# Kernel optimization log

Hardware: AMD Instinct MI355X
Metric: run time of the kernel (lower is better)

## Reference

```python
import jax, jax.numpy as jnp
import numpy as np

TOP_K = 2

def setup_inputs() -> dict:
    key = jax.random.key(0)
    ks = jax.random.split(key, 5)
    B, S, D, E, R, H = 4, 2048, 1024, 8, 128, 4096
    s = 0.02
    return {
        "hidden_states": jax.random.normal(ks[0], (B, S, D), jnp.float32),
        "w_route": jax.random.normal(ks[1], (E, D, R), jnp.float32) * s,
        "w3": jax.random.normal(ks[2], (E, D, H), jnp.float32) * s,
        "wr2h": jax.random.normal(ks[3], (E, R, H), jnp.float32) * s,
        "wh2d": jax.random.normal(ks[4], (E, H, D), jnp.float32) * s,
    }

def reference(hidden_states, w_route, w3, wr2h, wh2d):
    B, S, D = hidden_states.shape
    E = w_route.shape[0]
    x = hidden_states.reshape(-1, D)                      # [N, D]
    N = x.shape[0]
    # per-expert routing activations (also reused as w1_state inside experts)
    acts = jnp.einsum('nd,edr->ner', x, w_route)          # [N, E, R]
    norms = jnp.linalg.norm(acts, axis=-1)                # [N, E] router logits
    probs = jax.nn.softmax(norms.astype(jnp.float32), axis=-1)
    topw, sel = jax.lax.top_k(probs, TOP_K)               # [N, k]
    topw = topw / topw.sum(axis=-1, keepdims=True)
    topw = topw.astype(x.dtype)
    # dense combine weights: routing weight if expert selected, else 0
    combine = jnp.zeros((N, E), x.dtype).at[jnp.arange(N)[:, None], sel].add(topw)
    out = jnp.zeros_like(x)
    for e in range(E):  # fixed small expert count
        h = (x @ w3[e]) * jax.nn.silu(acts[:, e, :] @ wr2h[e])  # [N, H]
        out = out + (h @ wh2d[e]) * combine[:, e:e + 1]
    final = out.reshape(B, S, D)
    # load balancing loss on the router logits (expert_act_norms)
    mask = jax.nn.one_hot(sel, E, dtype=jnp.float32)      # [N, k, E]
    tokens_per_expert = mask.mean(axis=0)                 # [k, E]
    router_prob_per_expert = probs.mean(axis=0)           # [E]
    bl_loss = jnp.sum(tokens_per_expert * router_prob_per_expert[None, :]) * E
    return final, norms, bl_loss
```

## Files before the change

### kernel.cpp

```cpp
#include <hip/hip_runtime.h>


#define DEV static __device__ __forceinline__

typedef float  f32x4  __attribute__((ext_vector_type(4)));
typedef __bf16 bf16x8 __attribute__((ext_vector_type(8)));

DEV unsigned short f2bf(float f) {
  union { float f; unsigned u; } v; v.f = f;
  unsigned r = v.u + 0x7fffu + ((v.u >> 16) & 1u);
  return (unsigned short)(r >> 16);
}
DEV float bf2f(unsigned short b) {
  union { unsigned u; float f; } v; v.u = ((unsigned)b) << 16;
  return v.f;
}

DEV void gll16(const void* g, void* l) {
  __builtin_amdgcn_global_load_lds(
      (const __attribute__((address_space(1))) unsigned int*)g,
      (__attribute__((address_space(3))) unsigned int*)l, 16, 0, 0);
}

DEV f32x4 mfma16(bf16x8 a, bf16x8 b, f32x4 c) {
  return __builtin_amdgcn_mfma_f32_16x16x32_bf16(a, b, c, 0, 0, 0);
}

DEV int xcd_swz_gen(int bid, int nwg) {
  int x = bid & 7, o = bid >> 3;
  int q = nwg >> 3, r = nwg & 7;
  return (x < r ? x * (q + 1) : r * (q + 1) + (x - r) * q) + o;
}

DEV bf16x8 frag_read(const unsigned short* lds, int row, int kb) {
  int off = row * 128 + ((kb * 2) ^ ((row & 7) << 4));
  return *(const bf16x8*)((const char*)lds + off);
}

DEV void stage_linear(const unsigned short* base, size_t pitch, int k0,
                      unsigned short* lds, int tid) {
  int wq = tid >> 6, lane = tid & 63;
#pragma unroll
  for (int i = 0; i < 4; ++i) {
    int s = wq * 256 + i * 64 + lane;
    int row = s >> 3, b = s & 7;
    int bb = b ^ (row & 7);
    const unsigned short* g = base + (size_t)row * pitch + (size_t)(k0 + bb * 8);
    gll16(g, lds + (size_t)(wq * 256 + i * 64) * 8);
  }
}

DEV void stage_l256(const unsigned short* base, size_t pitch, int k0,
                    unsigned short* lds, int tid) {
  int wq = tid >> 6, lane = tid & 63;
#pragma unroll
  for (int i = 0; i < 4; ++i) {
    int sb = wq * 256 + i * 64;
    int s = sb + lane;
    int row = s >> 3, b = s & 7;
    int bb = b ^ (row & 7);
    gll16(base + (size_t)row * pitch + (size_t)(k0 + bb * 8),
          lds + (size_t)sb * 8);
  }
}
DEV void stage_g256(const unsigned short* base, size_t pitch, size_t colOff,
                    int k0, const int* toks, unsigned short* lds, int tid) {
  int wq = tid >> 6, lane = tid & 63;
#pragma unroll
  for (int i = 0; i < 4; ++i) {
    int sb = wq * 256 + i * 64;
    int s = sb + lane;
    int row = s >> 3, b = s & 7;
    int bb = b ^ (row & 7);
    gll16(base + (size_t)toks[row] * pitch + colOff + (size_t)(k0 + bb * 8),
          lds + (size_t)sb * 8);
  }
}
DEV void stage_l128(const unsigned short* base, size_t pitch, int k0,
                    unsigned short* lds, int tid) {
  int wq = tid >> 6, lane = tid & 63;
#pragma unroll
  for (int i = 0; i < 2; ++i) {
    int sb = wq * 128 + i * 64;
    int s = sb + lane;
    int row = s >> 3, b = s & 7;
    int bb = b ^ (row & 7);
    gll16(base + (size_t)row * pitch + (size_t)(k0 + bb * 8),
          lds + (size_t)sb * 8);
  }
}

DEV void mfma_block(const unsigned short* A, const unsigned short* B,
                    f32x4 (&acc)[4][4], int wm, int wn, int lg, int lc) {
#pragma unroll
  for (int ks = 0; ks < 2; ++ks) {
    int kb = ks * 32 + lg * 8;
    bf16x8 af[4], bff[4];
#pragma unroll
    for (int i = 0; i < 4; ++i) {
      af[i]  = frag_read(A, wm * 64 + i * 16 + lc, kb);
      bff[i] = frag_read(B, wn * 64 + i * 16 + lc, kb);
    }
#pragma unroll
    for (int mf = 0; mf < 4; ++mf)
#pragma unroll
      for (int nf = 0; nf < 4; ++nf)
        acc[mf][nf] = mfma16(af[mf], bff[nf], acc[mf][nf]);
  }
}
DEV void mfma256x256(const unsigned short* A, const unsigned short* B,
                     f32x4 (&acc)[8][4], int wm, int wn, int lg, int lc) {
#pragma unroll
  for (int ks = 0; ks < 2; ++ks) {
    int kb = ks * 32 + lg * 8;
    bf16x8 af[8], bff[4];
#pragma unroll
    for (int i = 0; i < 8; ++i) af[i] = frag_read(A, wm * 128 + i * 16 + lc, kb);
#pragma unroll
    for (int i = 0; i < 4; ++i) bff[i] = frag_read(B, wn * 64 + i * 16 + lc, kb);
#pragma unroll
    for (int mf = 0; mf < 8; ++mf)
#pragma unroll
      for (int nf = 0; nf < 4; ++nf)
        acc[mf][nf] = mfma16(af[mf], bff[nf], acc[mf][nf]);
  }
}
DEV void mfma256x128(const unsigned short* A, const unsigned short* B,
                     f32x4 (&acc)[8][2], int wm, int wn, int lg, int lc) {
#pragma unroll
  for (int ks = 0; ks < 2; ++ks) {
    int kb = ks * 32 + lg * 8;
    bf16x8 af[8], bff[2];
#pragma unroll
    for (int i = 0; i < 8; ++i) af[i] = frag_read(A, wm * 128 + i * 16 + lc, kb);
#pragma unroll
    for (int i = 0; i < 2; ++i) bff[i] = frag_read(B, wn * 32 + i * 16 + lc, kb);
#pragma unroll
    for (int mf = 0; mf < 8; ++mf)
#pragma unroll
      for (int nf = 0; nf < 2; ++nf)
        acc[mf][nf] = mfma16(af[mf], bff[nf], acc[mf][nf]);
  }
}


__global__ __launch_bounds__(256) void k_cast_x(const float* __restrict__ x,
    unsigned short* __restrict__ xh, unsigned short* __restrict__ xl) {
  int stride = gridDim.x * blockDim.x;
  for (int i = blockIdx.x * blockDim.x + threadIdx.x; i < 8192 * 1024 / 4;
       i += stride) {
    float4 v = ((const float4*)x)[i];
    ushort4 h, l;
    h.x = f2bf(v.x); l.x = f2bf(v.x - bf2f(h.x));
    h.y = f2bf(v.y); l.y = f2bf(v.y - bf2f(h.y));
    h.z = f2bf(v.z); l.z = f2bf(v.z - bf2f(h.z));
    h.w = f2bf(v.w); l.w = f2bf(v.w - bf2f(h.w));
    ((ushort4*)xh)[i] = h;
    ((ushort4*)xl)[i] = l;
  }
}

__global__ void k_zero(int* cnt, float* probsum) {
  int t = threadIdx.x;
  if (t < 16) cnt[t] = 0;
  if (t < 8)  probsum[t] = 0.f;
}

__global__ __launch_bounds__(256) void k_transp(const float* __restrict__ src,
    unsigned short* __restrict__ dst, int K, int N) {
  int ntn = N >> 6;
  int kt = blockIdx.x / ntn, nt = blockIdx.x % ntn;
  int e = blockIdx.y;
  __shared__ float tl[64][65];
  const float* s = src + (size_t)e * K * N;
  unsigned short* d = dst + (size_t)e * N * K;
  int tid = threadIdx.x;
  int c4 = (tid & 15) * 4, rr = tid >> 4;
#pragma unroll
  for (int p = 0; p < 4; ++p) {
    int row = rr + p * 16;
    float4 v = *(const float4*)(s + (size_t)(kt * 64 + row) * N + nt * 64 + c4);
    tl[row][c4] = v.x; tl[row][c4 + 1] = v.y;
    tl[row][c4 + 2] = v.z; tl[row][c4 + 3] = v.w;
  }
  __syncthreads();
#pragma unroll
  for (int p = 0; p < 4; ++p) {
    int n = rr + p * 16;
    ushort4 o;
    o.x = f2bf(tl[c4 + 0][n]); o.y = f2bf(tl[c4 + 1][n]);
    o.z = f2bf(tl[c4 + 2][n]); o.w = f2bf(tl[c4 + 3][n]);
    *(ushort4*)(d + (size_t)(nt * 64 + n) * K + kt * 64 + c4) = o;
  }
}

__global__ __launch_bounds__(256) void k_transp_split(const float* __restrict__ src,
    unsigned short* __restrict__ dh, unsigned short* __restrict__ dl, int K, int N) {
  int ntn = N >> 6;
  int kt = blockIdx.x / ntn, nt = blockIdx.x % ntn;
  int e = blockIdx.y;
  __shared__ float tl[64][65];
  const float* s = src + (size_t)e * K * N;
  size_t dbase = (size_t)e * N * K;
  int tid = threadIdx.x;
  int c4 = (tid & 15) * 4, rr = tid >> 4;
#pragma unroll
  for (int p = 0; p < 4; ++p) {
    int row = rr + p * 16;
    float4 v = *(const float4*)(s + (size_t)(kt * 64 + row) * N + nt * 64 + c4);
    tl[row][c4] = v.x; tl[row][c4 + 1] = v.y;
    tl[row][c4 + 2] = v.z; tl[row][c4 + 3] = v.w;
  }
  __syncthreads();
#pragma unroll
  for (int p = 0; p < 4; ++p) {
    int n = rr + p * 16;
    ushort4 oh, ol;
#pragma unroll
    for (int i = 0; i < 4; ++i) {
      float v = tl[c4 + i][n];
      unsigned short hh = f2bf(v);
      unsigned short ll = f2bf(v - bf2f(hh));
      ((unsigned short*)&oh)[i] = hh;
      ((unsigned short*)&ol)[i] = ll;
    }
    *(ushort4*)(dh + dbase + (size_t)(nt * 64 + n) * K + kt * 64 + c4) = oh;
    *(ushort4*)(dl + dbase + (size_t)(nt * 64 + n) * K + kt * 64 + c4) = ol;
  }
}

__global__ __launch_bounds__(256) void k_route_gemm(
    const unsigned short* __restrict__ xh, const unsigned short* __restrict__ xl,
    const unsigned short* __restrict__ wrh_t, const unsigned short* __restrict__ wrl_t,
    unsigned short* __restrict__ acts, float* __restrict__ norms_out) {
  __shared__ __align__(16) unsigned short Ah[128 * 64], Al[128 * 64];
  __shared__ __align__(16) unsigned short Bh[128 * 64], Bl[128 * 64];
  __shared__ float ssq_s[128][2];
  int tid = threadIdx.x;
  int mt = blockIdx.x, e = blockIdx.y;
  int wq = tid >> 6, lane = tid & 63;
  int wm = wq >> 1, wn = wq & 1, lg = lane >> 4, lc = lane & 15;
  f32x4 acc[4][4] = {};
  const unsigned short* ah_src = xh + (size_t)mt * 128 * 1024;
  const unsigned short* al_src = xl + (size_t)mt * 128 * 1024;
  const unsigned short* bh_src = wrh_t + (size_t)e * 128 * 1024;
  const unsigned short* bl_src = wrl_t + (size_t)e * 128 * 1024;
  for (int kt = 0; kt < 16; ++kt) {
    int k0 = kt * 64;
    stage_linear(ah_src, 1024, k0, Ah, tid);
    stage_linear(al_src, 1024, k0, Al, tid);
    stage_linear(bh_src, 1024, k0, Bh, tid);
    stage_linear(bl_src, 1024, k0, Bl, tid);
    __syncthreads();
#pragma unroll
    for (int ks = 0; ks < 2; ++ks) {
      int kb = ks * 32 + lg * 8;
      bf16x8 ahf[4], alf[4], bhf[4], blf[4];
#pragma unroll
      for (int i = 0; i < 4; ++i) {
        ahf[i] = frag_read(Ah, wm * 64 + i * 16 + lc, kb);
        alf[i] = frag_read(Al, wm * 64 + i * 16 + lc, kb);
        bhf[i] = frag_read(Bh, wn * 64 + i * 16 + lc, kb);
        blf[i] = frag_read(Bl, wn * 64 + i * 16 + lc, kb);
      }
#pragma unroll
      for (int mf = 0; mf < 4; ++mf)
#pragma unroll
        for (int nf = 0; nf < 4; ++nf) {
          acc[mf][nf] = mfma16(ahf[mf], bhf[nf], acc[mf][nf]);
          acc[mf][nf] = mfma16(alf[mf], bhf[nf], acc[mf][nf]);
          acc[mf][nf] = mfma16(ahf[mf], blf[nf], acc[mf][nf]);
        }
    }
    __syncthreads();
  }
  float ssq[4][4];
#pragma unroll
  for (int mf = 0; mf < 4; ++mf)
#pragma unroll
    for (int r = 0; r < 4; ++r) ssq[mf][r] = 0.f;
#pragma unroll
  for (int mf = 0; mf < 4; ++mf)
#pragma unroll
    for (int nf = 0; nf < 4; ++nf)
#pragma unroll
      for (int r = 0; r < 4; ++r) {
        float v = acc[mf][nf][r];
        int row = wm * 64 + mf * 16 + lg * 4 + r;
        int col = wn * 64 + nf * 16 + lc;
        acts[(size_t)(mt * 128 + row) * 1024 + e * 128 + col] = f2bf(v);
        ssq[mf][r] += v * v;
      }
#pragma unroll
  for (int mf = 0; mf < 4; ++mf)
#pragma unroll
    for (int r = 0; r < 4; ++r) {
      float s = ssq[mf][r];
      s += __shfl_xor(s, 1); s += __shfl_xor(s, 2);
      s += __shfl_xor(s, 4); s += __shfl_xor(s, 8);
      if (lc == 0) ssq_s[wm * 64 + mf * 16 + lg * 4 + r][wn] = s;
    }
  __syncthreads();
  if (tid < 128) {
    float s = ssq_s[tid][0] + ssq_s[tid][1];
    norms_out[(size_t)(mt * 128 + tid) * 8 + e] = sqrtf(s);
  }
}

__global__ __launch_bounds__(256) void k_router(const float* __restrict__ norms,
    float* __restrict__ topw, int* __restrict__ sel,
    int* __restrict__ cnt, float* __restrict__ probsum) {
  __shared__ float ps_s[8];
  __shared__ int cnt_s[16];
  int tid = threadIdx.x;
  if (tid < 8)  ps_s[tid] = 0.f;
  if (tid < 16) cnt_s[tid] = 0;
  __syncthreads();
  int n = blockIdx.x * 256 + tid;
  float p[8], mx = -3.4e38f;
#pragma unroll
  for (int e = 0; e < 8; ++e) { p[e] = norms[(size_t)n * 8 + e]; mx = fmaxf(mx, p[e]); }
  float s = 0.f;
#pragma unroll
  for (int e = 0; e < 8; ++e) { p[e] = __expf(p[e] - mx); s += p[e]; }
  float inv = 1.f / s;
  int i1 = 0; float v1 = p[0];
#pragma unroll
  for (int e = 1; e < 8; ++e) if (p[e] > v1) { v1 = p[e]; i1 = e; }
  int i2 = -1; float v2 = -1.f;
#pragma unroll
  for (int e = 0; e < 8; ++e) if (e != i1 && p[e] > v2) { v2 = p[e]; i2 = e; }
  float wsum = v1 + v2;
  topw[n * 2 + 0] = v1 / wsum;
  topw[n * 2 + 1] = v2 / wsum;
  sel[n * 2 + 0] = i1;
  sel[n * 2 + 1] = i2;
  atomicAdd(&cnt_s[i1], 1);
  atomicAdd(&cnt_s[8 + i2], 1);
#pragma unroll
  for (int e = 0; e < 8; ++e) atomicAdd(&ps_s[e], p[e] * inv);
  __syncthreads();
  if (tid < 8)  atomicAdd(&probsum[tid], ps_s[tid]);
  if (tid < 16) atomicAdd(&cnt[tid], cnt_s[tid]);
}

__global__ void k_plan(const int* __restrict__ cnt, const float* __restrict__ probsum,
                       int* __restrict__ offs, int* __restrict__ fill,
                       int4* __restrict__ tilemap, float* __restrict__ bl_out) {
  int t = 0;
  for (int k = 0; k < 2; ++k) {
    int pos = 0;
    for (int e = 0; e < 8; ++e) {
      int c = cnt[k * 8 + e];
      offs[k * 8 + e] = pos;
      int ntl = (c + 255) >> 8;
      for (int i = 0; i < ntl; ++i) {
        int rr = c - i * 256; if (rr > 256) rr = 256;
        tilemap[t] = make_int4(e, k * 8192 + pos + i * 256, rr, 0);
        ++t;
      }
      pos += c;
    }
  }
  for (; t < 80; ++t) tilemap[t] = make_int4(0, 0, 0, 0);
  for (int i = 0; i < 16; ++i) fill[i] = 0;
  float bl = 0.f;
  for (int e = 0; e < 8; ++e)
    bl += ((float)(cnt[e] + cnt[8 + e]) / 8192.f) * (probsum[e] / 8192.f);
  *bl_out = bl * 8.f;
}

__global__ __launch_bounds__(256) void k_fill(const int* __restrict__ sel,
    const float* __restrict__ topw, const int* __restrict__ offs,
    int* __restrict__ fill, int* __restrict__ list01, float* __restrict__ wlist) {
  int n = blockIdx.x * 256 + threadIdx.x;
#pragma unroll
  for (int k = 0; k < 2; ++k) {
    int e = sel[n * 2 + k];
    int pos = atomicAdd(&fill[k * 8 + e], 1);
    int idx = k * 8192 + offs[k * 8 + e] + pos;
    list01[idx] = n;
    wlist[idx] = topw[n * 2 + k];
  }
}

__global__ __launch_bounds__(512, 2) void k_gemm1(
    const unsigned short* __restrict__ xh, const unsigned short* __restrict__ acts,
    const unsigned short* __restrict__ w3t, const unsigned short* __restrict__ wr2h_t,
    const int* __restrict__ list, const int4* __restrict__ tilemap, int tile_lo,
    int nt, unsigned short* __restrict__ hbuf) {
  __shared__ __align__(16) unsigned short SA[2][256 * 64];
  __shared__ __align__(16) unsigned short SB[2][128 * 64];
  __shared__ int toks[256];
  int wg = xcd_swz_gen((int)blockIdx.x, nt * 32);
  int tloc = wg >> 5, bn = wg & 31;
  int4 ent = tilemap[tile_lo + tloc];
  int e = ent.x, posbase = ent.y, rows = ent.z;
  if (rows == 0) return;
  int tid = threadIdx.x;
  if (tid < 256) {
    int rr = tid < rows ? tid : rows - 1;
    toks[tid] = list[posbase + rr];
  }
  __syncthreads();
  int wq = tid >> 6, lane = tid & 63;
  int wm = wq >> 2, wn = wq & 3, lg = lane >> 4, lc = lane & 15;
  f32x4 acc_a[8][2] = {}, acc_s[8][2] = {};
  const unsigned short* bsrc  = w3t + ((size_t)e * 4096 + bn * 128) * 1024;
  const unsigned short* b2src = wr2h_t + ((size_t)e * 4096 + bn * 128) * 128;
  stage_g256(xh, 1024, 0, 0, toks, SA[0], tid);
  stage_l128(bsrc, 1024, 0, SB[0], tid);
  __syncthreads();
  int cur = 0;
  for (int kt = 0; kt < 15; ++kt) {
    stage_g256(xh, 1024, 0, (kt + 1) * 64, toks, SA[cur ^ 1], tid);
    stage_l128(bsrc, 1024, (kt + 1) * 64, SB[cur ^ 1], tid);
    mfma256x128(SA[cur], SB[cur], acc_a, wm, wn, lg, lc);
    __syncthreads();
    cur ^= 1;
  }
  stage_g256(acts, 1024, (size_t)e * 128, 0, toks, SA[cur ^ 1], tid);
  stage_l128(b2src, 128, 0, SB[cur ^ 1], tid);
  mfma256x128(SA[cur], SB[cur], acc_a, wm, wn, lg, lc);
  __syncthreads();
  cur ^= 1;
  stage_g256(acts, 1024, (size_t)e * 128, 64, toks, SA[cur ^ 1], tid);
  stage_l128(b2src, 128, 64, SB[cur ^ 1], tid);
  mfma256x128(SA[cur], SB[cur], acc_s, wm, wn, lg, lc);
  __syncthreads();
  cur ^= 1;
  mfma256x128(SA[cur], SB[cur], acc_s, wm, wn, lg, lc);
  size_t hrow0 = (size_t)tloc * 256;
#pragma unroll
  for (int mf = 0; mf < 8; ++mf)
#pragma unroll
    for (int nf = 0; nf < 2; ++nf)
#pragma unroll
      for (int r = 0; r < 4; ++r) {
        int row = wm * 128 + mf * 16 + lg * 4 + r;
        if (row < rows) {
          int col = wn * 32 + nf * 16 + lc;
          float sv = acc_s[mf][nf][r];
          float hv = acc_a[mf][nf][r] * (sv / (1.f + __expf(-sv)));
          hbuf[(hrow0 + row) * 4096 + (size_t)bn * 128 + col] = f2bf(hv);
        }
      }
}

__global__ __launch_bounds__(512, 2) void k_gemm2(
    const unsigned short* __restrict__ hbuf, const unsigned short* __restrict__ wh2dt,
    const int* __restrict__ list, const float* __restrict__ wlist,
    const int4* __restrict__ tilemap, int tile_lo, int nt,
    float* __restrict__ out) {
  __shared__ __align__(16) unsigned short SA[2][256 * 64];
  __shared__ __align__(16) unsigned short SB[2][256 * 64];
  __shared__ int toks[256];
  __shared__ float wr_s[256];
  int wg = xcd_swz_gen((int)blockIdx.x, nt * 4);
  int tloc = wg >> 2, bn = wg & 3;
  int4 ent = tilemap[tile_lo + tloc];
  int e = ent.x, posbase = ent.y, rows = ent.z;
  if (rows == 0) return;
  int tid = threadIdx.x;
  if (tid < 256) {
    int rr = tid < rows ? tid : rows - 1;
    int t = list[posbase + rr];
    toks[tid] = t;
    wr_s[tid] = wlist[posbase + rr];
  }
  __syncthreads();
  int wq = tid >> 6, lane = tid & 63;
  int wm = wq >> 2, wn = wq & 3, lg = lane >> 4, lc = lane & 15;
  f32x4 acc[8][4] = {};
  const unsigned short* asrc = hbuf + (size_t)tloc * 256 * 4096;
  const unsigned short* bsrc = wh2dt + ((size_t)e * 1024 + bn * 256) * 4096;
  stage_l256(asrc, 4096, 0, SA[0], tid);
  stage_l256(bsrc, 4096, 0, SB[0], tid);
  __syncthreads();
  int cur = 0;
  for (int kt = 0; kt < 63; ++kt) {
    stage_l256(asrc, 4096, (kt + 1) * 64, SA[cur ^ 1], tid);
    stage_l256(bsrc, 4096, (kt + 1) * 64, SB[cur ^ 1], tid);
    mfma256x256(SA[cur], SB[cur], acc, wm, wn, lg, lc);
    __syncthreads();
    cur ^= 1;
  }
  mfma256x256(SA[cur], SB[cur], acc, wm, wn, lg, lc);
#pragma unroll
  for (int mf = 0; mf < 8; ++mf)
#pragma unroll
    for (int nf = 0; nf < 4; ++nf)
#pragma unroll
      for (int r = 0; r < 4; ++r) {
        int row = wm * 128 + mf * 16 + lg * 4 + r;
        if (row < rows) {
          int col = wn * 64 + nf * 16 + lc;
          float v = acc[mf][nf][r] * wr_s[row];
          atomicAdd(out + (size_t)toks[row] * 1024 + bn * 256 + col, v);
        }
      }
}


extern "C" void kernel_launch(void* const* d_in, const int* in_sizes, int n_in,
                              void* d_out, int out_size, void* d_ws, size_t ws_size,
                              hipStream_t stream) {
  (void)in_sizes; (void)n_in; (void)out_size;
  const float* x      = (const float*)d_in[0];
  const float* wroute = (const float*)d_in[1];
  const float* w3     = (const float*)d_in[2];
  const float* wr2h   = (const float*)d_in[3];
  const float* wh2d   = (const float*)d_in[4];
  float* out = (float*)d_out;

  char* ws = (char*)d_ws;
  size_t off = 0;
  auto carve = [&](size_t bytes) -> void* {
    void* p = ws + off; off += (bytes + 255) & ~(size_t)255; return p;
  };
  unsigned short* xh     = (unsigned short*)carve((size_t)8192 * 1024 * 2);
  unsigned short* xl     = (unsigned short*)carve((size_t)8192 * 1024 * 2);
  unsigned short* wrh_t  = (unsigned short*)carve((size_t)8 * 128 * 1024 * 2);
  unsigned short* wrl_t  = (unsigned short*)carve((size_t)8 * 128 * 1024 * 2);
  unsigned short* w3t    = (unsigned short*)carve((size_t)8 * 4096 * 1024 * 2);
  unsigned short* wr2h_t = (unsigned short*)carve((size_t)8 * 4096 * 128 * 2);
  unsigned short* wh2dt  = (unsigned short*)carve((size_t)8 * 1024 * 4096 * 2);
  unsigned short* acts   = (unsigned short*)carve((size_t)8192 * 1024 * 2);
  int*   list01 = (int*)carve(2 * 8192 * 4);
  float* wlist  = (float*)carve(2 * 8192 * 4);
  int*   sel    = (int*)carve(8192 * 2 * 4);
  float* topw   = (float*)carve(8192 * 2 * 4);
  int*   ctr    = (int*)carve(8192);
  int* cnt = ctr; int* fill = ctr + 16; int* offs = ctr + 32;
  float* probsum = (float*)(ctr + 48);
  int4* tilemap = (int4*)(ctr + 64);

  size_t avail = ws_size > off ? ws_size - off : 0;
  int tpc = 0;
  const int cands[4] = {80, 40, 20, 10};
  for (int i = 0; i < 4; ++i) {
    if ((size_t)cands[i] * 256 * 4096 * 2 <= avail) { tpc = cands[i]; break; }
  }
  if (!tpc) return;
  unsigned short* hbuf = (unsigned short*)(ws + off);

  float* norms_out = out + 8388608;
  float* bl_out    = out + 8454144;

  hipMemsetAsync(out, 0, (size_t)8388608 * 4, stream);
  k_cast_x<<<2048, 256, 0, stream>>>(x, xh, xl);
  k_zero<<<1, 64, 0, stream>>>(cnt, probsum);
  k_transp<<<dim3(16 * 64, 8), 256, 0, stream>>>(w3, w3t, 1024, 4096);
  k_transp<<<dim3(64 * 16, 8), 256, 0, stream>>>(wh2d, wh2dt, 4096, 1024);
  k_transp<<<dim3(2 * 64, 8), 256, 0, stream>>>(wr2h, wr2h_t, 128, 4096);
  k_transp_split<<<dim3(16 * 2, 8), 256, 0, stream>>>(wroute, wrh_t, wrl_t, 1024, 128);
  k_route_gemm<<<dim3(64, 8), 256, 0, stream>>>(xh, xl, wrh_t, wrl_t, acts, norms_out);
  k_router<<<32, 256, 0, stream>>>(norms_out, topw, sel, cnt, probsum);
  k_plan<<<1, 1, 0, stream>>>(cnt, probsum, offs, fill, tilemap, bl_out);
  k_fill<<<32, 256, 0, stream>>>(sel, topw, offs, fill, list01, wlist);

  int nchunk = (80 + tpc - 1) / tpc;
  for (int c = 0; c < nchunk; ++c) {
    int tile_lo = c * tpc;
    int nt = 80 - tile_lo < tpc ? 80 - tile_lo : tpc;
    k_gemm1<<<nt * 32, 512, 0, stream>>>(
        xh, acts, w3t, wr2h_t, list01, tilemap, tile_lo, nt, hbuf);
    k_gemm2<<<nt * 4, 512, 0, stream>>>(
        hbuf, wh2dt, list01, wlist, tilemap, tile_lo, nt, out);
  }
}
```

Measured before the change: 955.0 us.

## Restructure expert GEMMs into quadrant-interleaved pipelines with fine-grained waitcnt

Rewrites the main loops of both expert GEMM kernels (gated up-projection and down-projection) as an explicit software pipeline. Each tile is split into quadrants whose LDS fragment reads, global-to-LDS stages and MFMA blocks are interleaved. Full __syncthreads are replaced by s_barrier plus manual vmcnt/lgkmcnt waits and s_setprio around the MFMA bursts. The per-warp tile mapping changes to a 2x2 quadrant layout. The goal is to hide global load latency and LDS traffic behind matrix math, at the cost of fragile hand-counted wait counts and more complex scheduling.

```diff
diff --git a/kernel.cpp b/kernel.cpp
--- a/kernel.cpp
+++ b/kernel.cpp
@@ -5,6 +5,10 @@
 
 typedef float  f32x4  __attribute__((ext_vector_type(4)));
 typedef __bf16 bf16x8 __attribute__((ext_vector_type(8)));
+
+#define VMCNT_(n) asm volatile("s_waitcnt vmcnt(" #n ")" ::: "memory")
+#define VMCNT(n) VMCNT_(n)
+#define LGKM0()  asm volatile("s_waitcnt lgkmcnt(0)" ::: "memory")
 
 DEV unsigned short f2bf(float f) {
   union { float f; unsigned u; } v; v.f = f;
@@ -49,47 +53,6 @@
     gll16(g, lds + (size_t)(wq * 256 + i * 64) * 8);
   }
 }
-
-DEV void stage_l256(const unsigned short* base, size_t pitch, int k0,
-                    unsigned short* lds, int tid) {
-  int wq = tid >> 6, lane = tid & 63;
-#pragma unroll
-  for (int i = 0; i < 4; ++i) {
-    int sb = wq * 256 + i * 64;
-    int s = sb + lane;
-    int row = s >> 3, b = s & 7;
-    int bb = b ^ (row & 7);
-    gll16(base + (size_t)row * pitch + (size_t)(k0 + bb * 8),
-          lds + (size_t)sb * 8);
-  }
-}
-DEV void stage_g256(const unsigned short* base, size_t pitch, size_t colOff,
-                    int k0, const int* toks, unsigned short* lds, int tid) {
-  int wq = tid >> 6, lane = tid & 63;
-#pragma unroll
-  for (int i = 0; i < 4; ++i) {
-    int sb = wq * 256 + i * 64;
-    int s = sb + lane;
-    int row = s >> 3, b = s & 7;
-    int bb = b ^ (row & 7);
-    gll16(base + (size_t)toks[row] * pitch + colOff + (size_t)(k0 + bb * 8),
-          lds + (size_t)sb * 8);
-  }
-}
-DEV void stage_l128(const unsigned short* base, size_t pitch, int k0,
-                    unsigned short* lds, int tid) {
-  int wq = tid >> 6, lane = tid & 63;
-#pragma unroll
-  for (int i = 0; i < 2; ++i) {
-    int sb = wq * 128 + i * 64;
-    int s = sb + lane;
-    int row = s >> 3, b = s & 7;
-    int bb = b ^ (row & 7);
-    gll16(base + (size_t)row * pitch + (size_t)(k0 + bb * 8),
-          lds + (size_t)sb * 8);
-  }
-}
-
 DEV void mfma_block(const unsigned short* A, const unsigned short* B,
                     f32x4 (&acc)[4][4], int wm, int wn, int lg, int lc) {
 #pragma unroll
@@ -105,40 +68,6 @@
     for (int mf = 0; mf < 4; ++mf)
 #pragma unroll
       for (int nf = 0; nf < 4; ++nf)
-        acc[mf][nf] = mfma16(af[mf], bff[nf], acc[mf][nf]);
-  }
-}
-DEV void mfma256x256(const unsigned short* A, const unsigned short* B,
-                     f32x4 (&acc)[8][4], int wm, int wn, int lg, int lc) {
-#pragma unroll
-  for (int ks = 0; ks < 2; ++ks) {
-    int kb = ks * 32 + lg * 8;
-    bf16x8 af[8], bff[4];
-#pragma unroll
-    for (int i = 0; i < 8; ++i) af[i] = frag_read(A, wm * 128 + i * 16 + lc, kb);
-#pragma unroll
-    for (int i = 0; i < 4; ++i) bff[i] = frag_read(B, wn * 64 + i * 16 + lc, kb);
-#pragma unroll
-    for (int mf = 0; mf < 8; ++mf)
-#pragma unroll
-      for (int nf = 0; nf < 4; ++nf)
-        acc[mf][nf] = mfma16(af[mf], bff[nf], acc[mf][nf]);
-  }
-}
-DEV void mfma256x128(const unsigned short* A, const unsigned short* B,
-                     f32x4 (&acc)[8][2], int wm, int wn, int lg, int lc) {
-#pragma unroll
-  for (int ks = 0; ks < 2; ++ks) {
-    int kb = ks * 32 + lg * 8;
-    bf16x8 af[8], bff[2];
-#pragma unroll
-    for (int i = 0; i < 8; ++i) af[i] = frag_read(A, wm * 128 + i * 16 + lc, kb);
-#pragma unroll
-    for (int i = 0; i < 2; ++i) bff[i] = frag_read(B, wn * 32 + i * 16 + lc, kb);
-#pragma unroll
-    for (int mf = 0; mf < 8; ++mf)
-#pragma unroll
-      for (int nf = 0; nf < 2; ++nf)
         acc[mf][nf] = mfma16(af[mf], bff[nf], acc[mf][nf]);
   }
 }
@@ -405,46 +334,134 @@
   __syncthreads();
   int wq = tid >> 6, lane = tid & 63;
   int wm = wq >> 2, wn = wq & 3, lg = lane >> 4, lc = lane & 15;
-  f32x4 acc_a[8][2] = {}, acc_s[8][2] = {};
-  const unsigned short* bsrc  = w3t + ((size_t)e * 4096 + bn * 128) * 1024;
-  const unsigned short* b2src = wr2h_t + ((size_t)e * 4096 + bn * 128) * 128;
-  stage_g256(xh, 1024, 0, 0, toks, SA[0], tid);
-  stage_l128(bsrc, 1024, 0, SB[0], tid);
-  __syncthreads();
-  int cur = 0;
-  for (int kt = 0; kt < 15; ++kt) {
-    stage_g256(xh, 1024, 0, (kt + 1) * 64, toks, SA[cur ^ 1], tid);
-    stage_l128(bsrc, 1024, (kt + 1) * 64, SB[cur ^ 1], tid);
-    mfma256x128(SA[cur], SB[cur], acc_a, wm, wn, lg, lc);
-    __syncthreads();
-    cur ^= 1;
-  }
-  stage_g256(acts, 1024, (size_t)e * 128, 0, toks, SA[cur ^ 1], tid);
-  stage_l128(b2src, 128, 0, SB[cur ^ 1], tid);
-  mfma256x128(SA[cur], SB[cur], acc_a, wm, wn, lg, lc);
-  __syncthreads();
-  cur ^= 1;
-  stage_g256(acts, 1024, (size_t)e * 128, 64, toks, SA[cur ^ 1], tid);
-  stage_l128(b2src, 128, 64, SB[cur ^ 1], tid);
-  mfma256x128(SA[cur], SB[cur], acc_s, wm, wn, lg, lc);
-  __syncthreads();
-  cur ^= 1;
-  mfma256x128(SA[cur], SB[cur], acc_s, wm, wn, lg, lc);
+
+  int sa0 = tid, sa1 = tid + 512;
+  int ra0 = sa0 >> 3, ra1 = sa1 >> 3;
+  int ca0 = ((sa0 & 7) ^ (ra0 & 7)) * 8;
+  int ca1 = ((sa1 & 7) ^ (ra1 & 7)) * 8;
+  int tA00 = toks[ra0],      tA01 = toks[128 + ra0];
+  int tA10 = toks[ra1],      tA11 = toks[128 + ra1];
+  int rb = tid >> 3;
+  int cb = ((tid & 7) ^ (rb & 7)) * 8;
+
+  auto stageA = [&](int t, int h, int bi) {
+    unsigned short* d0 = &SA[bi][(size_t)(h * 1024 + sa0) * 8];
+    unsigned short* d1 = &SA[bi][(size_t)(h * 1024 + sa1) * 8];
+    int t0 = h ? tA01 : tA00, t1 = h ? tA11 : tA10;
+    if (t < 16) {
+      int k0 = t * 64;
+      gll16(xh + (size_t)t0 * 1024 + k0 + ca0, d0);
+      gll16(xh + (size_t)t1 * 1024 + k0 + ca1, d1);
+    } else {
+      int k0 = e * 128 + (t - 16) * 64;
+      gll16(acts + (size_t)t0 * 1024 + k0 + ca0, d0);
+      gll16(acts + (size_t)t1 * 1024 + k0 + ca1, d1);
+    }
+  };
+  auto stageB = [&](int t, int h, int bi) {
+    unsigned short* d = &SB[bi][(size_t)(h * 512 + tid) * 8];
+    if (t < 16) {
+      gll16(w3t + ((size_t)e * 4096 + bn * 128 + h * 64 + rb) * 1024 + t * 64 + cb, d);
+    } else {
+      gll16(wr2h_t + ((size_t)e * 4096 + bn * 128 + h * 64 + rb) * 128 +
+                (t - 16) * 64 + cb, d);
+    }
+  };
+
+  f32x4 accm[2][4][2] = {}, accg[2][4][2] = {};
+  bf16x8 af[4][2], bf[2][2];
+
+#define G1_RA(BI, QM)                                                        \
+  _Pragma("unroll") for (int mf = 0; mf < 4; ++mf)                           \
+  _Pragma("unroll") for (int ks = 0; ks < 2; ++ks)                           \
+    af[mf][ks] = frag_read(SA[BI], QM * 128 + wm * 64 + mf * 16 + lc,        \
+                           ks * 32 + lg * 8);
+#define G1_RB(BI, QN)                                                        \
+  _Pragma("unroll") for (int ks = 0; ks < 2; ++ks)                           \
+    bf[QN][ks] = frag_read(SB[BI], QN * 64 + wn * 16 + lc, ks * 32 + lg * 8);
+#define G1_MMA(ACC, QM, QN)                                                  \
+  __builtin_amdgcn_s_barrier();                                              \
+  LGKM0();                                                                   \
+  __builtin_amdgcn_s_setprio(1);                                             \
+  _Pragma("unroll") for (int mf = 0; mf < 4; ++mf)                           \
+  _Pragma("unroll") for (int ks = 0; ks < 2; ++ks)                           \
+    ACC[QM][mf][QN] = mfma16(af[mf][ks], bf[QN][ks], ACC[QM][mf][QN]);       \
+  __builtin_amdgcn_s_setprio(0);                                             \
+  __builtin_amdgcn_s_barrier();
+
+  stageA(0, 0, 0); stageB(0, 0, 0); stageB(0, 1, 0); stageA(0, 1, 0);
+  stageA(1, 0, 1); stageB(1, 0, 1); stageB(1, 1, 1);
+  VMCNT(4);
+  __builtin_amdgcn_s_barrier();
+
+  for (int it = 0; it < 8; ++it) {
+    int t0 = 2 * it;
+    G1_RA(0, 0); G1_RB(0, 0);
+    stageA(t0 + 1, 1, 1);
+    G1_MMA(accm, 0, 0);
+    G1_RB(0, 1);
+    stageA(t0 + 2, 0, 0);
+    G1_MMA(accm, 0, 1);
+    G1_RA(0, 1);
+    stageB(t0 + 2, 0, 0);
+    G1_MMA(accm, 1, 1);
+    stageB(t0 + 2, 1, 0);
+    VMCNT(4);
+    G1_MMA(accm, 1, 0);
+    G1_RA(1, 0); G1_RB(1, 0);
+    stageA(t0 + 2, 1, 0);
+    G1_MMA(accm, 0, 0);
+    G1_RB(1, 1);
+    stageA(t0 + 3, 0, 1);
+    G1_MMA(accm, 0, 1);
+    G1_RA(1, 1);
+    stageB(t0 + 3, 0, 1);
+    G1_MMA(accm, 1, 1);
+    stageB(t0 + 3, 1, 1);
+    VMCNT(4);
+    G1_MMA(accm, 1, 0);
+  }
+  {
+    G1_RA(0, 0); G1_RB(0, 0);
+    stageA(17, 1, 1);
+    G1_MMA(accg, 0, 0);
+    G1_RB(0, 1);
+    G1_MMA(accg, 0, 1);
+    G1_RA(0, 1);
+    G1_MMA(accg, 1, 1);
+    VMCNT(3);
+    G1_MMA(accg, 1, 0);
+    G1_RA(1, 0); G1_RB(1, 0);
+    VMCNT(2);
+    G1_MMA(accg, 0, 0);
+    G1_RB(1, 1);
+    VMCNT(0);
+    G1_MMA(accg, 0, 1);
+    G1_RA(1, 1);
+    G1_MMA(accg, 1, 1);
+    G1_MMA(accg, 1, 0);
+  }
+#undef G1_RA
+#undef G1_RB
+#undef G1_MMA
+
   size_t hrow0 = (size_t)tloc * 256;
 #pragma unroll
-  for (int mf = 0; mf < 8; ++mf)
-#pragma unroll
-    for (int nf = 0; nf < 2; ++nf)
-#pragma unroll
-      for (int r = 0; r < 4; ++r) {
-        int row = wm * 128 + mf * 16 + lg * 4 + r;
-        if (row < rows) {
-          int col = wn * 32 + nf * 16 + lc;
-          float sv = acc_s[mf][nf][r];
-          float hv = acc_a[mf][nf][r] * (sv / (1.f + __expf(-sv)));
-          hbuf[(hrow0 + row) * 4096 + (size_t)bn * 128 + col] = f2bf(hv);
+  for (int qm = 0; qm < 2; ++qm)
+#pragma unroll
+    for (int mf = 0; mf < 4; ++mf)
+#pragma unroll
+      for (int qn = 0; qn < 2; ++qn)
+#pragma unroll
+        for (int r = 0; r < 4; ++r) {
+          int row = qm * 128 + wm * 64 + mf * 16 + lg * 4 + r;
+          if (row < rows) {
+            int col = qn * 64 + wn * 16 + lc;
+            float sv = accg[qm][mf][qn][r];
+            float hv = accm[qm][mf][qn][r] * (sv / (1.f + __expf(-sv)));
+            hbuf[(hrow0 + row) * 4096 + (size_t)bn * 128 + col] = f2bf(hv);
+          }
         }
-      }
 }
 
 __global__ __launch_bounds__(512, 2) void k_gemm2(
@@ -464,41 +481,131 @@
   int tid = threadIdx.x;
   if (tid < 256) {
     int rr = tid < rows ? tid : rows - 1;
-    int t = list[posbase + rr];
-    toks[tid] = t;
+    toks[tid] = list[posbase + rr];
     wr_s[tid] = wlist[posbase + rr];
   }
   __syncthreads();
   int wq = tid >> 6, lane = tid & 63;
   int wm = wq >> 2, wn = wq & 3, lg = lane >> 4, lc = lane & 15;
-  f32x4 acc[8][4] = {};
-  const unsigned short* asrc = hbuf + (size_t)tloc * 256 * 4096;
-  const unsigned short* bsrc = wh2dt + ((size_t)e * 1024 + bn * 256) * 4096;
-  stage_l256(asrc, 4096, 0, SA[0], tid);
-  stage_l256(bsrc, 4096, 0, SB[0], tid);
-  __syncthreads();
-  int cur = 0;
-  for (int kt = 0; kt < 63; ++kt) {
-    stage_l256(asrc, 4096, (kt + 1) * 64, SA[cur ^ 1], tid);
-    stage_l256(bsrc, 4096, (kt + 1) * 64, SB[cur ^ 1], tid);
-    mfma256x256(SA[cur], SB[cur], acc, wm, wn, lg, lc);
-    __syncthreads();
-    cur ^= 1;
-  }
-  mfma256x256(SA[cur], SB[cur], acc, wm, wn, lg, lc);
-#pragma unroll
-  for (int mf = 0; mf < 8; ++mf)
-#pragma unroll
-    for (int nf = 0; nf < 4; ++nf)
-#pragma unroll
-      for (int r = 0; r < 4; ++r) {
-        int row = wm * 128 + mf * 16 + lg * 4 + r;
-        if (row < rows) {
-          int col = wn * 64 + nf * 16 + lc;
-          float v = acc[mf][nf][r] * wr_s[row];
-          atomicAdd(out + (size_t)toks[row] * 1024 + bn * 256 + col, v);
-        }
-      }
+
+  int sa0 = tid, sa1 = tid + 512;
+  int ra0 = sa0 >> 3, ra1 = sa1 >> 3;
+  int ca0 = ((sa0 & 7) ^ (ra0 & 7)) * 8;
+  int ca1 = ((sa1 & 7) ^ (ra1 & 7)) * 8;
+  const unsigned short* abase = hbuf + (size_t)tloc * 256 * 4096;
+  const unsigned short* bbase = wh2dt + ((size_t)e * 1024 + bn * 256) * 4096;
+
+  auto stageA = [&](int t, int h, int bi) {
+    gll16(abase + (size_t)(h * 128 + ra0) * 4096 + t * 64 + ca0,
+          &SA[bi][(size_t)(h * 1024 + sa0) * 8]);
+    gll16(abase + (size_t)(h * 128 + ra1) * 4096 + t * 64 + ca1,
+          &SA[bi][(size_t)(h * 1024 + sa1) * 8]);
+  };
+  auto stageB = [&](int t, int h, int bi) {
+    gll16(bbase + (size_t)(h * 128 + ra0) * 4096 + t * 64 + ca0,
+          &SB[bi][(size_t)(h * 1024 + sa0) * 8]);
+    gll16(bbase + (size_t)(h * 128 + ra1) * 4096 + t * 64 + ca1,
+          &SB[bi][(size_t)(h * 1024 + sa1) * 8]);
+  };
+
+  f32x4 acc[2][4][2][2] = {};
+  bf16x8 af[4][2], bf[2][2][2];
+
+#define G2_RA(BI, QM)                                                        \
+  _Pragma("unroll") for (int mf = 0; mf < 4; ++mf)                           \
+  _Pragma("unroll") for (int ks = 0; ks < 2; ++ks)                           \
+    af[mf][ks] = frag_read(SA[BI], QM * 128 + wm * 64 + mf * 16 + lc,        \
+                           ks * 32 + lg * 8);
+#define G2_RB(BI, QN)                                                        \
+  _Pragma("unroll") for (int nf = 0; nf < 2; ++nf)                           \
+  _Pragma("unroll") for (int ks = 0; ks < 2; ++ks)                           \
+    bf[QN][nf][ks] = frag_read(SB[BI], QN * 128 + wn * 32 + nf * 16 + lc,    \
+                               ks * 32 + lg * 8);
+#define G2_MMA(QM, QN)                                                       \
+  __builtin_amdgcn_s_barrier();                                              \
+  LGKM0();                                                                   \
+  __builtin_amdgcn_s_setprio(1);                                             \
+  _Pragma("unroll") for (int mf = 0; mf < 4; ++mf)                           \
+  _Pragma("unroll") for (int nf = 0; nf < 2; ++nf)                           \
+  _Pragma("unroll") for (int ks = 0; ks < 2; ++ks)                           \
+    acc[QM][mf][QN][nf] =                                                    \
+        mfma16(af[mf][ks], bf[QN][nf][ks], acc[QM][mf][QN][nf]);             \
+  __builtin_amdgcn_s_setprio(0);                                             \
+  __builtin_amdgcn_s_barrier();
+
+  stageA(0, 0, 0); stageB(0, 0, 0); stageB(0, 1, 0); stageA(0, 1, 0);
+  stageA(1, 0, 1); stageB(1, 0, 1); stageB(1, 1, 1);
+  VMCNT(6);
+  __builtin_amdgcn_s_barrier();
+
+  for (int it = 0; it < 31; ++it) {
+    int t0 = 2 * it;
+    G2_RA(0, 0); G2_RB(0, 0);
+    stageA(t0 + 1, 1, 1);
+    G2_MMA(0, 0);
+    G2_RB(0, 1);
+    stageA(t0 + 2, 0, 0);
+    G2_MMA(0, 1);
+    G2_RA(0, 1);
+    stageB(t0 + 2, 0, 0);
+    G2_MMA(1, 1);
+    stageB(t0 + 2, 1, 0);
+    VMCNT(6);
+    G2_MMA(1, 0);
+    G2_RA(1, 0); G2_RB(1, 0);
+    stageA(t0 + 2, 1, 0);
+    G2_MMA(0, 0);
+    G2_RB(1, 1);
+    stageA(t0 + 3, 0, 1);
+    G2_MMA(0, 1);
+    G2_RA(1, 1);
+    stageB(t0 + 3, 0, 1);
+    G2_MMA(1, 1);
+    stageB(t0 + 3, 1, 1);
+    VMCNT(6);
+    G2_MMA(1, 0);
+  }
+  {
+    G2_RA(0, 0); G2_RB(0, 0);
+    stageA(63, 1, 1);
+    G2_MMA(0, 0);
+    G2_RB(0, 1);
+    G2_MMA(0, 1);
+    G2_RA(0, 1);
+    G2_MMA(1, 1);
+    VMCNT(4);
+    G2_MMA(1, 0);
+    G2_RA(1, 0); G2_RB(1, 0);
+    VMCNT(2);
+    G2_MMA(0, 0);
+    G2_RB(1, 1);
+    VMCNT(0);
+    G2_MMA(0, 1);
+    G2_RA(1, 1);
+    G2_MMA(1, 1);
+    G2_MMA(1, 0);
+  }
+#undef G2_RA
+#undef G2_RB
+#undef G2_MMA
+
+#pragma unroll
+  for (int qm = 0; qm < 2; ++qm)
+#pragma unroll
+    for (int mf = 0; mf < 4; ++mf)
+#pragma unroll
+      for (int qn = 0; qn < 2; ++qn)
+#pragma unroll
+        for (int nf = 0; nf < 2; ++nf)
+#pragma unroll
+          for (int r = 0; r < 4; ++r) {
+            int row = qm * 128 + wm * 64 + mf * 16 + lg * 4 + r;
+            if (row < rows) {
+              int col = qn * 128 + wn * 32 + nf * 16 + lc;
+              float v = acc[qm][mf][qn][nf][r] * wr_s[row];
+              atomicAdd(out + (size_t)toks[row] * 1024 + bn * 256 + col, v);
+            }
+          }
 }
 
 
```

Measured after the change: 844.0 us. 11.6% less time.
